# Optimization experiments

Hardware: AMD Instinct MI355X
Metric: run time of the kernel (lower is better)

## Reference

```python
import jax, jax.numpy as jnp
import numpy as np

N_NODES = 50000
N_EDGES = 800000
IN_FEATS = 128
N_HIDDEN = 128
N_CLASSES = 16


def setup_inputs() -> dict:
    key = jax.random.key(0)
    ks = jax.random.split(key, 10)
    d = {
        'x': jax.random.normal(ks[0], (N_NODES, IN_FEATS), dtype=jnp.float32),
        'src': jax.random.randint(ks[1], (N_EDGES,), 0, N_NODES, dtype=jnp.int32),
        'dst': jax.random.randint(ks[2], (N_EDGES,), 0, N_NODES, dtype=jnp.int32),
    }
    sc = 1.0 / np.sqrt(N_HIDDEN)
    d['w_self0'] = jax.random.normal(ks[3], (IN_FEATS, N_HIDDEN), dtype=jnp.float32) * sc
    d['w_neigh0'] = jax.random.normal(ks[4], (IN_FEATS, N_HIDDEN), dtype=jnp.float32) * sc
    d['b0'] = jnp.zeros((N_HIDDEN,), dtype=jnp.float32)
    d['w_self1'] = jax.random.normal(ks[5], (N_HIDDEN, N_HIDDEN), dtype=jnp.float32) * sc
    d['w_neigh1'] = jax.random.normal(ks[6], (N_HIDDEN, N_HIDDEN), dtype=jnp.float32) * sc
    d['b1'] = jnp.zeros((N_HIDDEN,), dtype=jnp.float32)
    d['w_self2'] = jax.random.normal(ks[7], (N_HIDDEN, N_HIDDEN), dtype=jnp.float32) * sc
    d['w_neigh2'] = jax.random.normal(ks[8], (N_HIDDEN, N_HIDDEN), dtype=jnp.float32) * sc
    d['b2'] = jnp.zeros((N_HIDDEN,), dtype=jnp.float32)
    d['w_head'] = jax.random.normal(ks[9], (N_HIDDEN, N_CLASSES), dtype=jnp.float32) * sc
    d['b_head'] = jnp.zeros((N_CLASSES,), dtype=jnp.float32)
    return d


def _sage_conv(h, src, dst, inv_deg, w_self, w_neigh, b):
    # mean aggregator: gather src features, scatter-add to dst, divide by in-degree
    agg = jax.ops.segment_sum(h[src], dst, num_segments=N_NODES)  # [N, d]
    neigh = agg * inv_deg[:, None]
    return h @ w_self + neigh @ w_neigh + b


def reference(x, src, dst, w_self0, w_neigh0, b0, w_self1, w_neigh1, b1,
              w_self2, w_neigh2, b2, w_head, b_head):
    deg = jax.ops.segment_sum(jnp.ones((src.shape[0],), jnp.float32), dst,
                              num_segments=N_NODES)
    inv_deg = 1.0 / jnp.maximum(deg, 1.0)
    h = x  # dropout is identity in eval mode
    for (ws, wn, b) in ((w_self0, w_neigh0, b0),
                        (w_self1, w_neigh1, b1),
                        (w_self2, w_neigh2, b2)):
        h = jax.nn.relu(_sage_conv(h, src, dst, inv_deg, ws, wn, b))
    pls = jnp.mean(h, axis=0, keepdims=True)  # AvgPooling over single graph -> [1, n_hidden]
    score = pls @ w_head + b_head  # [1, n_classes]
    return (score, pls)
```

## Files before the change

kernel.cpp:

```cpp
#include <hip/hip_runtime.h>
#include <hip/hip_bf16.h>
#include <stdint.h>

#define NN 50000
#define NE 800000
#define F 128
#define NCLS 16
#define NB 196
#define BCAP 5120
#define PA_EPT 16

typedef __attribute__((ext_vector_type(8))) short short8;
typedef __attribute__((ext_vector_type(4))) float f32x4;
typedef __attribute__((ext_vector_type(4))) unsigned int uint4v;

#define OB_COLSUM    0u
#define OB_BCUR      512u
#define OB_BBASE     1536u
#define OB_ROWSTART  4096u
#define OB_INVDEG    208896u
#define OB_PAIRS     409600u
#define OB_SRCS16    4423680u
#define OB_WT        6023680u
#define OB_XB        6220800u
#define OB_HB1       19020800u
#define OB_NB2       31820800u

__device__ __forceinline__ uint32_t swz_off(uint32_t row, uint32_t k) {
    uint32_t c = ((k >> 5) << 2) | ((k >> 2) & 3u);
    uint32_t b = (((k >> 4) & 1u) << 3) | ((k & 3u) << 1);
    return (row << 8) + (((c ^ (row & 15u)) << 4) | b);
}

__device__ __forceinline__ float bf_lo(uint32_t d) { return __uint_as_float(d << 16); }
__device__ __forceinline__ float bf_hi(uint32_t d) { return __uint_as_float(d & 0xffff0000u); }
__device__ __forceinline__ uint32_t pack_bf2(float a, float b) {
    __hip_bfloat16 l = __float2bfloat16(a), h = __float2bfloat16(b);
    return ((uint32_t)(*(uint16_t*)&h) << 16) | (uint32_t)(*(uint16_t*)&l);
}

__global__ void init_kernel(float* __restrict__ colsum, int* __restrict__ bcur) {
    int t = threadIdx.x;
    if (t < 128) colsum[t] = 0.f;
    if (t < NB) bcur[t] = t * BCAP;
}

__global__ __launch_bounds__(256) void convert_x(const float* __restrict__ x,
                                                 uint8_t* __restrict__ xb) {
    int t = blockIdx.x * 256 + threadIdx.x;
    uint32_t row = (uint32_t)t >> 5;
    uint32_t q = (uint32_t)t & 31u;
    float4 v = *(const float4*)(x + row * F + q * 4);
    uint32_t c = ((q >> 3) << 2) | (q & 3u);
    uint32_t hi = (q >> 2) & 1u;
    uint2 pk;
    pk.x = pack_bf2(v.x, v.y);
    pk.y = pack_bf2(v.z, v.w);
    *(uint2*)(xb + (row << 8) + (((c ^ (row & 15u)) << 4) | (hi << 3))) = pk;
}

__global__ __launch_bounds__(256) void prep_w(const float* __restrict__ w0, const float* __restrict__ w1,
                                              const float* __restrict__ w2, const float* __restrict__ w3,
                                              const float* __restrict__ w4, const float* __restrict__ w5,
                                              uint8_t* __restrict__ wt) {
    int m = blockIdx.y;
    const float* w = m == 0 ? w0 : m == 1 ? w1 : m == 2 ? w2 : m == 3 ? w3 : m == 4 ? w4 : w5;
    int t = blockIdx.x * 256 + threadIdx.x;
    int n = t >> 6;
    int k0 = (t & 63) << 1;
    uint32_t pk = pack_bf2(w[k0 * F + n], w[(k0 + 1) * F + n]);
    *(uint32_t*)(wt + (uint32_t)m * 32768u + swz_off((uint32_t)n, (uint32_t)k0)) = pk;
}

__global__ __launch_bounds__(256) void pass_a(const int* __restrict__ src,
                                              const int* __restrict__ dst,
                                              int* __restrict__ bcur,
                                              uint32_t* __restrict__ pairs) {
    __shared__ int cnt[NB];
    __shared__ int base_s[NB];
    int t = threadIdx.x;
    for (int i = t; i < NB; i += 256) cnt[i] = 0;
    __syncthreads();

    uint32_t pk[PA_EPT];
    int bk[PA_EPT];
    int e0 = blockIdx.x * (256 * PA_EPT) + t;
#pragma unroll
    for (int j = 0; j < PA_EPT; ++j) {
        int e = e0 + j * 256;
        if (e < NE) {
            int sv = src[e], dv = dst[e];
            bk[j] = dv >> 8;
            pk[j] = (uint32_t)sv | (((uint32_t)dv & 255u) << 16);
            atomicAdd(&cnt[bk[j]], 1);
        } else bk[j] = -1;
    }
    __syncthreads();
    for (int i = t; i < NB; i += 256) {
        if (cnt[i] > 0) base_s[i] = atomicAdd(&bcur[i], cnt[i]);
        cnt[i] = 0;
    }
    __syncthreads();
#pragma unroll
    for (int j = 0; j < PA_EPT; ++j) {
        if (bk[j] >= 0) {
            int pos = base_s[bk[j]] + atomicAdd(&cnt[bk[j]], 1);
            pairs[pos] = pk[j];
        }
    }
}

__global__ __launch_bounds__(256) void bucket_scan(const int* __restrict__ bcur,
                                                   int* __restrict__ bbase,
                                                   int* __restrict__ row_start) {
    __shared__ int s[256];
    int t = threadIdx.x;
    int fill = (t < NB) ? (bcur[t] - t * BCAP) : 0;
    s[t] = fill;
    __syncthreads();
    for (int off = 1; off < 256; off <<= 1) {
        int u = (t >= off) ? s[t - off] : 0;
        __syncthreads();
        s[t] += u;
        __syncthreads();
    }
    if (t < NB) bbase[t] = s[t] - fill;
    if (t == 0) row_start[NN] = NE;
}

__global__ __launch_bounds__(256) void pass_b(const uint32_t* __restrict__ pairs,
                                              const int* __restrict__ bcur,
                                              const int* __restrict__ bbase,
                                              int* __restrict__ row_start,
                                              float* __restrict__ inv_deg,
                                              unsigned short* __restrict__ srcs) {
    __shared__ int cnt[256];
    __shared__ int s[256];
    __shared__ int cur[256];
    int b = blockIdx.x, t = threadIdx.x;
    int in0 = b * BCAP;
    int fill = bcur[b] - in0;
    int out0 = bbase[b];
    cnt[t] = 0;
    __syncthreads();
    for (int i = t; i < fill; i += 256)
        atomicAdd(&cnt[pairs[in0 + i] >> 16], 1);
    __syncthreads();
    int v = cnt[t];
    s[t] = v;
    __syncthreads();
    for (int off = 1; off < 256; off <<= 1) {
        int u = (t >= off) ? s[t - off] : 0;
        __syncthreads();
        s[t] += u;
        __syncthreads();
    }
    int excl = s[t] - v;
    cur[t] = out0 + excl;
    int row = (b << 8) + t;
    if (row < NN) {
        row_start[row] = out0 + excl;
        inv_deg[row] = 1.0f / (float)(v > 1 ? v : 1);
    }
    __syncthreads();
    for (int i = t; i < fill; i += 256) {
        uint32_t p = pairs[in0 + i];
        int pos = atomicAdd(&cur[p >> 16], 1);
        srcs[pos] = (unsigned short)(p & 0xffffu);
    }
}

__global__ __launch_bounds__(256) void aggregate_b(
        const uint8_t* __restrict__ hb, const int* __restrict__ row_start,
        const unsigned short* __restrict__ srcs, const float* __restrict__ inv_deg,
        uint8_t* __restrict__ nb) {
    int node = blockIdx.x * 4 + (threadIdx.x >> 6);
    int l = threadIdx.x & 63;
    int half = l >> 5;
    uint32_t sub = (uint32_t)(l & 31);
    uint32_t c_lin = sub & 15u;
    uint32_t boff = (sub >> 4) << 3;
    int e0 = row_start[node], e1 = row_start[node + 1];
    float a0 = 0.f, a1 = 0.f, a2 = 0.f, a3 = 0.f;

#define LDROW(S) (*(const uint2*)(hb + ((uint32_t)(S) << 8) + (((c_lin ^ ((uint32_t)(S) & 15u)) << 4) | boff)))
    int e = e0 + half;
    for (; e + 6 < e1; e += 8) {
        uint32_t s0 = srcs[e], s1 = srcs[e + 2], s2 = srcs[e + 4], s3 = srcs[e + 6];
        uint2 d0 = LDROW(s0);
        uint2 d1 = LDROW(s1);
        uint2 d2 = LDROW(s2);
        uint2 d3 = LDROW(s3);
        a0 += bf_lo(d0.x) + bf_lo(d1.x) + bf_lo(d2.x) + bf_lo(d3.x);
        a1 += bf_hi(d0.x) + bf_hi(d1.x) + bf_hi(d2.x) + bf_hi(d3.x);
        a2 += bf_lo(d0.y) + bf_lo(d1.y) + bf_lo(d2.y) + bf_lo(d3.y);
        a3 += bf_hi(d0.y) + bf_hi(d1.y) + bf_hi(d2.y) + bf_hi(d3.y);
    }
    for (; e < e1; e += 2) {
        uint32_t s0 = srcs[e];
        uint2 d0 = LDROW(s0);
        a0 += bf_lo(d0.x); a1 += bf_hi(d0.x); a2 += bf_lo(d0.y); a3 += bf_hi(d0.y);
    }
#undef LDROW
    a0 += __shfl_xor(a0, 32);
    a1 += __shfl_xor(a1, 32);
    a2 += __shfl_xor(a2, 32);
    a3 += __shfl_xor(a3, 32);
    if (half == 0) {
        float idg = inv_deg[node];
        uint2 pk;
        pk.x = pack_bf2(a0 * idg, a1 * idg);
        pk.y = pack_bf2(a2 * idg, a3 * idg);
        *(uint2*)(nb + ((uint32_t)node << 8) +
                  (((c_lin ^ ((uint32_t)node & 15u)) << 4) | boff)) = pk;
    }
}

__global__ __launch_bounds__(256) void gemm_mfma(
        const uint8_t* __restrict__ a_self, const uint8_t* __restrict__ a_neigh,
        const uint8_t* __restrict__ wt_self, const uint8_t* __restrict__ wt_neigh,
        const float* __restrict__ bias, uint8_t* __restrict__ hout,
        float* colsum) {
    __shared__ uint4v As4[1024];
    __shared__ uint4v Ws4[2048];
    __shared__ float cs[128];
    int tid = threadIdx.x;
    int lane = tid & 63, wave = tid >> 6;
    int rl = lane & 15, g = lane >> 4;
    int row0 = blockIdx.x * 64;

    f32x4 acc[8];
    f32x4 z = {0.f, 0.f, 0.f, 0.f};
#pragma unroll
    for (int nt = 0; nt < 8; ++nt) acc[nt] = z;

    const char* AsB = (const char*)As4;
    const char* WsB = (const char*)Ws4;

#pragma unroll
    for (int pass = 0; pass < 2; ++pass) {
        if (pass) __syncthreads();
        const uint4v* ga = (const uint4v*)((pass ? a_neigh : a_self) + (size_t)row0 * 256);
        const uint4v* gw = (const uint4v*)(pass ? wt_neigh : wt_self);
#pragma unroll
        for (int i = 0; i < 4; ++i) As4[tid + i * 256] = ga[tid + i * 256];
#pragma unroll
        for (int i = 0; i < 8; ++i) Ws4[tid + i * 256] = gw[tid + i * 256];
        __syncthreads();
#pragma unroll
        for (int ks = 0; ks < 4; ++ks) {
            int chunk = ((ks << 2) | g) ^ rl;
            short8 a = *(const short8*)(AsB + ((wave * 16 + rl) << 8) + (chunk << 4));
#pragma unroll
            for (int nt = 0; nt < 8; ++nt) {
                short8 bb = *(const short8*)(WsB + ((nt * 16 + rl) << 8) + (chunk << 4));
                acc[nt] = __builtin_amdgcn_mfma_f32_16x16x32_bf16(a, bb, acc[nt], 0, 0, 0);
            }
        }
    }

    bool doCol = (colsum != nullptr);
    if (doCol) {
        if (tid < 128) cs[tid] = 0.f;
        __syncthreads();
    }
#pragma unroll
    for (int nt = 0; nt < 8; ++nt) {
        int col = nt * 16 + rl;
        float bv = bias[col];
        float rsum = 0.f;
#pragma unroll
        for (int i = 0; i < 4; ++i) {
            int row = row0 + wave * 16 + g * 4 + i;
            if (row < NN) {
                float v = fmaxf(acc[nt][i] + bv, 0.f);
                rsum += v;
                *(__hip_bfloat16*)(hout + swz_off((uint32_t)row, (uint32_t)col)) =
                    __float2bfloat16(v);
            }
        }
        if (doCol) atomicAdd(&cs[col], rsum);
    }
    if (doCol) {
        __syncthreads();
        if (tid < 128) atomicAdd(&colsum[tid], cs[tid]);
    }
}

__global__ __launch_bounds__(128) void head_kernel(const float* __restrict__ colsum,
                                                   const float* __restrict__ w_head,
                                                   const float* __restrict__ b_head,
                                                   float* __restrict__ out) {
    __shared__ float pls[F];
    int t = threadIdx.x;
    float p = colsum[t] * (1.0f / (float)NN);
    pls[t] = p;
    out[NCLS + t] = p;
    __syncthreads();
    if (t < NCLS) {
        float sc = b_head[t];
        for (int f = 0; f < F; ++f) sc += pls[f] * w_head[f * NCLS + t];
        out[t] = sc;
    }
}

extern "C" void kernel_launch(void* const* d_in, const int* in_sizes, int n_in,
                              void* d_out, int out_size, void* d_ws, size_t ws_size,
                              hipStream_t stream) {
    const float* x       = (const float*)d_in[0];
    const int*   src     = (const int*)d_in[1];
    const int*   dst     = (const int*)d_in[2];
    const float* w_self0 = (const float*)d_in[3];
    const float* w_neigh0= (const float*)d_in[4];
    const float* b0      = (const float*)d_in[5];
    const float* w_self1 = (const float*)d_in[6];
    const float* w_neigh1= (const float*)d_in[7];
    const float* b1      = (const float*)d_in[8];
    const float* w_self2 = (const float*)d_in[9];
    const float* w_neigh2= (const float*)d_in[10];
    const float* b2      = (const float*)d_in[11];
    const float* w_head  = (const float*)d_in[12];
    const float* b_head  = (const float*)d_in[13];
    float* out = (float*)d_out;

    uint8_t* ws = (uint8_t*)d_ws;
    float* colsum   = (float*)(ws + OB_COLSUM);
    int*   bcur     = (int*)(ws + OB_BCUR);
    int*   bbase    = (int*)(ws + OB_BBASE);
    int*   row_start= (int*)(ws + OB_ROWSTART);
    float* inv_deg  = (float*)(ws + OB_INVDEG);
    uint32_t* pairs = (uint32_t*)(ws + OB_PAIRS);
    unsigned short* srcs16 = (unsigned short*)(ws + OB_SRCS16);
    uint8_t* wt     = ws + OB_WT;
    uint8_t* xb     = ws + OB_XB;
    uint8_t* hb1    = ws + OB_HB1;
    uint8_t* nb     = ws + OB_NB2;

    init_kernel<<<1, 256, 0, stream>>>(colsum, bcur);
    convert_x<<<6250, 256, 0, stream>>>(x, xb);
    prep_w<<<dim3(32, 6), 256, 0, stream>>>(w_self0, w_neigh0, w_self1, w_neigh1,
                                            w_self2, w_neigh2, wt);
    pass_a<<<NB, 256, 0, stream>>>(src, dst, bcur, pairs);
    bucket_scan<<<1, 256, 0, stream>>>(bcur, bbase, row_start);
    pass_b<<<NB, 256, 0, stream>>>(pairs, bcur, bbase, row_start, inv_deg, srcs16);

    const int GB = (NN + 63) / 64;

    aggregate_b<<<12500, 256, 0, stream>>>(xb, row_start, srcs16, inv_deg, nb);
    gemm_mfma<<<GB, 256, 0, stream>>>(xb, nb, wt + 0 * 32768, wt + 1 * 32768, b0, hb1, nullptr);
    aggregate_b<<<12500, 256, 0, stream>>>(hb1, row_start, srcs16, inv_deg, nb);
    gemm_mfma<<<GB, 256, 0, stream>>>(hb1, nb, wt + 2 * 32768, wt + 3 * 32768, b1, xb, nullptr);
    aggregate_b<<<12500, 256, 0, stream>>>(xb, row_start, srcs16, inv_deg, nb);
    gemm_mfma<<<GB, 256, 0, stream>>>(xb, nb, wt + 4 * 32768, wt + 5 * 32768, b2, hb1, colsum);

    head_kernel<<<1, 128, 0, stream>>>(colsum, w_head, b_head, out);
}
```

Measured before the change: 220.1 us.

## Fuse neighbor aggregation into GEMM and gather from an FP8 feature copy

Merges the separate aggregate and GEMM kernels into one per-layer kernel. Each block gathers neighbor rows for its 64 nodes straight into shared memory, runs the neighbor GEMM, then loads the self features and runs the self GEMM. The gather now reads an extra FP8 (e4m3) row-major copy of the features, written by the previous layer's epilogue and by the input conversion. This halves the bytes pulled per edge and removes the round trip of the aggregated buffer through global memory. The cost is lower precision in the neighbor mean, extra FP8 byte stores in the epilogue, and a serial gather loop with fewer nodes in flight per wave, which may weaken latency hiding.

```diff
diff --git a/kernel.cpp b/kernel.cpp
--- a/kernel.cpp
+++ b/kernel.cpp
@@ -1,5 +1,6 @@
 #include <hip/hip_runtime.h>
 #include <hip/hip_bf16.h>
+#include <hip/hip_fp8.h>
 #include <stdint.h>
 
 #define NN 50000
@@ -12,19 +13,22 @@
 
 typedef __attribute__((ext_vector_type(8))) short short8;
 typedef __attribute__((ext_vector_type(4))) float f32x4;
+typedef __attribute__((ext_vector_type(2))) float f32x2;
 typedef __attribute__((ext_vector_type(4))) unsigned int uint4v;
 
 #define OB_COLSUM    0u
 #define OB_BCUR      512u
 #define OB_BBASE     1536u
 #define OB_ROWSTART  4096u
-#define OB_INVDEG    208896u
+#define OB_INVDEG    204800u
 #define OB_PAIRS     409600u
 #define OB_SRCS16    4423680u
 #define OB_WT        6023680u
 #define OB_XB        6220800u
 #define OB_HB1       19020800u
-#define OB_NB2       31820800u
+#define OB_X8        31820800u
+#define OB_F8A       38220800u
+#define OB_F8B       44620800u
 
 __device__ __forceinline__ uint32_t swz_off(uint32_t row, uint32_t k) {
     uint32_t c = ((k >> 5) << 2) | ((k >> 2) & 3u);
@@ -32,11 +36,42 @@
     return (row << 8) + (((c ^ (row & 15u)) << 4) | b);
 }
 
-__device__ __forceinline__ float bf_lo(uint32_t d) { return __uint_as_float(d << 16); }
-__device__ __forceinline__ float bf_hi(uint32_t d) { return __uint_as_float(d & 0xffff0000u); }
 __device__ __forceinline__ uint32_t pack_bf2(float a, float b) {
     __hip_bfloat16 l = __float2bfloat16(a), h = __float2bfloat16(b);
     return ((uint32_t)(*(uint16_t*)&h) << 16) | (uint32_t)(*(uint16_t*)&l);
+}
+
+__device__ __forceinline__ uint8_t f32_to_fp8(float v) {
+#if __has_builtin(__builtin_amdgcn_cvt_pk_fp8_f32)
+    return (uint8_t)(__builtin_amdgcn_cvt_pk_fp8_f32(v, 0.f, 0, false) & 0xff);
+#else
+    __hip_fp8_e4m3 t(v);
+    return t.__x;
+#endif
+}
+
+__device__ __forceinline__ uint32_t f32x4_to_fp8x4(float a, float b, float c, float d) {
+#if __has_builtin(__builtin_amdgcn_cvt_pk_fp8_f32)
+    int r = __builtin_amdgcn_cvt_pk_fp8_f32(a, b, 0, false);
+    r = __builtin_amdgcn_cvt_pk_fp8_f32(c, d, r, true);
+    return (uint32_t)r;
+#else
+    __hip_fp8_e4m3 ta(a), tb(b), tc(c), td(d);
+    return (uint32_t)ta.__x | ((uint32_t)tb.__x << 8) | ((uint32_t)tc.__x << 16) | ((uint32_t)td.__x << 24);
+#endif
+}
+
+__device__ __forceinline__ void fp8x4_to_f32(uint32_t d, float& f0, float& f1, float& f2, float& f3) {
+#if __has_builtin(__builtin_amdgcn_cvt_pk_f32_fp8)
+    f32x2 lo = __builtin_amdgcn_cvt_pk_f32_fp8((int)d, false);
+    f32x2 hi = __builtin_amdgcn_cvt_pk_f32_fp8((int)d, true);
+    f0 = lo.x; f1 = lo.y; f2 = hi.x; f3 = hi.y;
+#else
+    __hip_fp8_e4m3 t0, t1, t2, t3;
+    t0.__x = (uint8_t)(d & 0xff); t1.__x = (uint8_t)((d >> 8) & 0xff);
+    t2.__x = (uint8_t)((d >> 16) & 0xff); t3.__x = (uint8_t)((d >> 24) & 0xff);
+    f0 = (float)t0; f1 = (float)t1; f2 = (float)t2; f3 = (float)t3;
+#endif
 }
 
 __global__ void init_kernel(float* __restrict__ colsum, int* __restrict__ bcur) {
@@ -45,8 +80,9 @@
     if (t < NB) bcur[t] = t * BCAP;
 }
 
-__global__ __launch_bounds__(256) void convert_x(const float* __restrict__ x,
-                                                 uint8_t* __restrict__ xb) {
+__global__ __launch_bounds__(256) void convert_x2(const float* __restrict__ x,
+                                                  uint8_t* __restrict__ xb,
+                                                  uint8_t* __restrict__ x8) {
     int t = blockIdx.x * 256 + threadIdx.x;
     uint32_t row = (uint32_t)t >> 5;
     uint32_t q = (uint32_t)t & 31u;
@@ -57,6 +93,7 @@
     pk.x = pack_bf2(v.x, v.y);
     pk.y = pack_bf2(v.z, v.w);
     *(uint2*)(xb + (row << 8) + (((c ^ (row & 15u)) << 4) | (hi << 3))) = pk;
+    *(uint32_t*)(x8 + row * 128u + q * 4u) = f32x4_to_fp8x4(v.x, v.y, v.z, v.w);
 }
 
 __global__ __launch_bounds__(256) void prep_w(const float* __restrict__ w0, const float* __restrict__ w1,
@@ -170,92 +207,110 @@
     }
 }
 
-__global__ __launch_bounds__(256) void aggregate_b(
-        const uint8_t* __restrict__ hb, const int* __restrict__ row_start,
-        const unsigned short* __restrict__ srcs, const float* __restrict__ inv_deg,
-        uint8_t* __restrict__ nb) {
-    int node = blockIdx.x * 4 + (threadIdx.x >> 6);
-    int l = threadIdx.x & 63;
-    int half = l >> 5;
-    uint32_t sub = (uint32_t)(l & 31);
-    uint32_t c_lin = sub & 15u;
-    uint32_t boff = (sub >> 4) << 3;
-    int e0 = row_start[node], e1 = row_start[node + 1];
-    float a0 = 0.f, a1 = 0.f, a2 = 0.f, a3 = 0.f;
-
-#define LDROW(S) (*(const uint2*)(hb + ((uint32_t)(S) << 8) + (((c_lin ^ ((uint32_t)(S) & 15u)) << 4) | boff)))
-    int e = e0 + half;
-    for (; e + 6 < e1; e += 8) {
-        uint32_t s0 = srcs[e], s1 = srcs[e + 2], s2 = srcs[e + 4], s3 = srcs[e + 6];
-        uint2 d0 = LDROW(s0);
-        uint2 d1 = LDROW(s1);
-        uint2 d2 = LDROW(s2);
-        uint2 d3 = LDROW(s3);
-        a0 += bf_lo(d0.x) + bf_lo(d1.x) + bf_lo(d2.x) + bf_lo(d3.x);
-        a1 += bf_hi(d0.x) + bf_hi(d1.x) + bf_hi(d2.x) + bf_hi(d3.x);
-        a2 += bf_lo(d0.y) + bf_lo(d1.y) + bf_lo(d2.y) + bf_lo(d3.y);
-        a3 += bf_hi(d0.y) + bf_hi(d1.y) + bf_hi(d2.y) + bf_hi(d3.y);
-    }
-    for (; e < e1; e += 2) {
-        uint32_t s0 = srcs[e];
-        uint2 d0 = LDROW(s0);
-        a0 += bf_lo(d0.x); a1 += bf_hi(d0.x); a2 += bf_lo(d0.y); a3 += bf_hi(d0.y);
-    }
-#undef LDROW
-    a0 += __shfl_xor(a0, 32);
-    a1 += __shfl_xor(a1, 32);
-    a2 += __shfl_xor(a2, 32);
-    a3 += __shfl_xor(a3, 32);
-    if (half == 0) {
-        float idg = inv_deg[node];
-        uint2 pk;
-        pk.x = pack_bf2(a0 * idg, a1 * idg);
-        pk.y = pack_bf2(a2 * idg, a3 * idg);
-        *(uint2*)(nb + ((uint32_t)node << 8) +
-                  (((c_lin ^ ((uint32_t)node & 15u)) << 4) | boff)) = pk;
-    }
-}
-
-__global__ __launch_bounds__(256) void gemm_mfma(
-        const uint8_t* __restrict__ a_self, const uint8_t* __restrict__ a_neigh,
+__global__ __launch_bounds__(256) void sage_layer(
+        const uint8_t* __restrict__ hb16,
+        const uint8_t* __restrict__ hf8,
+        const int* __restrict__ row_start, const unsigned short* __restrict__ srcs,
+        const float* __restrict__ inv_deg,
         const uint8_t* __restrict__ wt_self, const uint8_t* __restrict__ wt_neigh,
-        const float* __restrict__ bias, uint8_t* __restrict__ hout,
+        const float* __restrict__ bias,
+        uint8_t* __restrict__ hout_b16, uint8_t* __restrict__ hout_f8,
         float* colsum) {
+    __shared__ uint4v Ws4[2048];
     __shared__ uint4v As4[1024];
-    __shared__ uint4v Ws4[2048];
     __shared__ float cs[128];
-    int tid = threadIdx.x;
-    int lane = tid & 63, wave = tid >> 6;
-    int rl = lane & 15, g = lane >> 4;
-    int row0 = blockIdx.x * 64;
+    const int tid = threadIdx.x;
+    const int lane = tid & 63, wave = tid >> 6;
+    const int rl = lane & 15, g = lane >> 4;
+    const int row0 = blockIdx.x * 64;
+    const char* AsB = (const char*)As4;
+    const char* WsB = (const char*)Ws4;
+
+    {
+        const uint4v* gw = (const uint4v*)wt_neigh;
+#pragma unroll
+        for (int i = 0; i < 8; ++i) Ws4[tid + i * 256] = gw[tid + i * 256];
+    }
+    {
+        int slot = lane >> 5;
+        uint32_t sub = (uint32_t)(lane & 31);
+        uint32_t c = ((sub >> 3) << 2) | (sub & 3u);
+        uint32_t hi8 = ((sub >> 2) & 1u) << 3;
+#pragma unroll 1
+        for (int r = 0; r < 8; ++r) {
+            int lr = wave * 16 + r * 2 + slot;
+            int node = row0 + lr;
+            bool valid = node < NN;
+            int e0 = valid ? row_start[node] : 0;
+            int e1 = valid ? row_start[node + 1] : 0;
+            float a0 = 0.f, a1 = 0.f, a2 = 0.f, a3 = 0.f;
+            int e = e0;
+            for (; e + 7 < e1; e += 8) {
+                uint32_t d[8];
+#pragma unroll
+                for (int j = 0; j < 8; ++j) {
+                    uint32_t s = srcs[e + j];
+                    d[j] = *(const uint32_t*)(hf8 + s * 128u + sub * 4u);
+                }
+#pragma unroll
+                for (int j = 0; j < 8; ++j) {
+                    float f0, f1, f2, f3;
+                    fp8x4_to_f32(d[j], f0, f1, f2, f3);
+                    a0 += f0; a1 += f1; a2 += f2; a3 += f3;
+                }
+            }
+            for (; e < e1; ++e) {
+                uint32_t s = srcs[e];
+                uint32_t dv = *(const uint32_t*)(hf8 + s * 128u + sub * 4u);
+                float f0, f1, f2, f3;
+                fp8x4_to_f32(dv, f0, f1, f2, f3);
+                a0 += f0; a1 += f1; a2 += f2; a3 += f3;
+            }
+            float idg = valid ? inv_deg[node] : 0.f;
+            uint2 pk;
+            pk.x = pack_bf2(a0 * idg, a1 * idg);
+            pk.y = pack_bf2(a2 * idg, a3 * idg);
+            *(uint2*)((char*)As4 + ((uint32_t)lr << 8) +
+                      (((c ^ ((uint32_t)lr & 15u)) << 4) | hi8)) = pk;
+        }
+    }
+    __syncthreads();
 
     f32x4 acc[8];
     f32x4 z = {0.f, 0.f, 0.f, 0.f};
 #pragma unroll
     for (int nt = 0; nt < 8; ++nt) acc[nt] = z;
 
-    const char* AsB = (const char*)As4;
-    const char* WsB = (const char*)Ws4;
-
-#pragma unroll
-    for (int pass = 0; pass < 2; ++pass) {
-        if (pass) __syncthreads();
-        const uint4v* ga = (const uint4v*)((pass ? a_neigh : a_self) + (size_t)row0 * 256);
-        const uint4v* gw = (const uint4v*)(pass ? wt_neigh : wt_self);
+#pragma unroll
+    for (int ks = 0; ks < 4; ++ks) {
+        int chunk = ((ks << 2) | g) ^ rl;
+        short8 a = *(const short8*)(AsB + ((wave * 16 + rl) << 8) + (chunk << 4));
+#pragma unroll
+        for (int nt = 0; nt < 8; ++nt) {
+            short8 bb = *(const short8*)(WsB + ((nt * 16 + rl) << 8) + (chunk << 4));
+            acc[nt] = __builtin_amdgcn_mfma_f32_16x16x32_bf16(a, bb, acc[nt], 0, 0, 0);
+        }
+    }
+    __syncthreads();
+
+    {
+        const uint4v* ga = (const uint4v*)(hb16 + (size_t)row0 * 256);
 #pragma unroll
         for (int i = 0; i < 4; ++i) As4[tid + i * 256] = ga[tid + i * 256];
+        const uint4v* gw = (const uint4v*)wt_self;
 #pragma unroll
         for (int i = 0; i < 8; ++i) Ws4[tid + i * 256] = gw[tid + i * 256];
-        __syncthreads();
-#pragma unroll
-        for (int ks = 0; ks < 4; ++ks) {
-            int chunk = ((ks << 2) | g) ^ rl;
-            short8 a = *(const short8*)(AsB + ((wave * 16 + rl) << 8) + (chunk << 4));
-#pragma unroll
-            for (int nt = 0; nt < 8; ++nt) {
-                short8 bb = *(const short8*)(WsB + ((nt * 16 + rl) << 8) + (chunk << 4));
-                acc[nt] = __builtin_amdgcn_mfma_f32_16x16x32_bf16(a, bb, acc[nt], 0, 0, 0);
-            }
+    }
+    __syncthreads();
+
+#pragma unroll
+    for (int ks = 0; ks < 4; ++ks) {
+        int chunk = ((ks << 2) | g) ^ rl;
+        short8 a = *(const short8*)(AsB + ((wave * 16 + rl) << 8) + (chunk << 4));
+#pragma unroll
+        for (int nt = 0; nt < 8; ++nt) {
+            short8 bb = *(const short8*)(WsB + ((nt * 16 + rl) << 8) + (chunk << 4));
+            acc[nt] = __builtin_amdgcn_mfma_f32_16x16x32_bf16(a, bb, acc[nt], 0, 0, 0);
         }
     }
 
@@ -275,8 +330,9 @@
             if (row < NN) {
                 float v = fmaxf(acc[nt][i] + bv, 0.f);
                 rsum += v;
-                *(__hip_bfloat16*)(hout + swz_off((uint32_t)row, (uint32_t)col)) =
+                *(__hip_bfloat16*)(hout_b16 + swz_off((uint32_t)row, (uint32_t)col)) =
                     __float2bfloat16(v);
+                hout_f8[(uint32_t)row * 128u + (uint32_t)col] = f32_to_fp8(v);
             }
         }
         if (doCol) atomicAdd(&cs[col], rsum);
@@ -334,10 +390,12 @@
     uint8_t* wt     = ws + OB_WT;
     uint8_t* xb     = ws + OB_XB;
     uint8_t* hb1    = ws + OB_HB1;
-    uint8_t* nb     = ws + OB_NB2;
+    uint8_t* x8     = ws + OB_X8;
+    uint8_t* f8a    = ws + OB_F8A;
+    uint8_t* f8b    = ws + OB_F8B;
 
     init_kernel<<<1, 256, 0, stream>>>(colsum, bcur);
-    convert_x<<<6250, 256, 0, stream>>>(x, xb);
+    convert_x2<<<6250, 256, 0, stream>>>(x, xb, x8);
     prep_w<<<dim3(32, 6), 256, 0, stream>>>(w_self0, w_neigh0, w_self1, w_neigh1,
                                             w_self2, w_neigh2, wt);
     pass_a<<<NB, 256, 0, stream>>>(src, dst, bcur, pairs);
@@ -346,12 +404,12 @@
 
     const int GB = (NN + 63) / 64;
 
-    aggregate_b<<<12500, 256, 0, stream>>>(xb, row_start, srcs16, inv_deg, nb);
-    gemm_mfma<<<GB, 256, 0, stream>>>(xb, nb, wt + 0 * 32768, wt + 1 * 32768, b0, hb1, nullptr);
-    aggregate_b<<<12500, 256, 0, stream>>>(hb1, row_start, srcs16, inv_deg, nb);
-    gemm_mfma<<<GB, 256, 0, stream>>>(hb1, nb, wt + 2 * 32768, wt + 3 * 32768, b1, xb, nullptr);
-    aggregate_b<<<12500, 256, 0, stream>>>(xb, row_start, srcs16, inv_deg, nb);
-    gemm_mfma<<<GB, 256, 0, stream>>>(xb, nb, wt + 4 * 32768, wt + 5 * 32768, b2, hb1, colsum);
+    sage_layer<<<GB, 256, 0, stream>>>(xb, x8, row_start, srcs16, inv_deg,
+                                       wt + 0 * 32768, wt + 1 * 32768, b0, hb1, f8a, nullptr);
+    sage_layer<<<GB, 256, 0, stream>>>(hb1, f8a, row_start, srcs16, inv_deg,
+                                       wt + 2 * 32768, wt + 3 * 32768, b1, xb, f8b, nullptr);
+    sage_layer<<<GB, 256, 0, stream>>>(xb, f8b, row_start, srcs16, inv_deg,
+                                       wt + 4 * 32768, wt + 5 * 32768, b2, hb1, f8a, colsum);
 
     head_kernel<<<1, 128, 0, stream>>>(colsum, w_head, b_head, out);
 }
```

Measured after the change: 328.6 us. 1.49x slower.
